# Performance work log

Hardware: AMD Instinct MI355X
Metric: run time of the kernel (lower is better)

Reference implementation:

```python
import jax, jax.numpy as jnp
import numpy as np

N = 10000      # nodes per graph
E = 160000     # random edges per graph (plus N self-loops)
IN_DIM = 4096
HID = 64       # num_hidden
H = 8          # heads
C = 5          # num_classes
SLOPE = 0.2    # LeakyReLU negative slope


def gat_conv(x, src, dst, W, al, ar, b, res_W=None):
    """DGL-style GATConv. x:(N,F) -> (N,H,D). Messages flow src->dst,
    edge softmax over in-edges of each dst node."""
    n = x.shape[0]
    h, d = al.shape
    feat = (x @ W).reshape(n, h, d)                      # (N,H,D)
    el = jnp.sum(feat * al, axis=-1)                     # (N,H)
    er = jnp.sum(feat * ar, axis=-1)                     # (N,H)
    e = jax.nn.leaky_relu(el[src] + er[dst], SLOPE)      # (E,H)
    emax = jax.ops.segment_max(e, dst, num_segments=n)   # (N,H) stable softmax
    ex = jnp.exp(e - emax[dst])
    denom = jax.ops.segment_sum(ex, dst, num_segments=n)
    alpha = ex / denom[dst]                              # (E,H)
    out = jax.ops.segment_sum(feat[src] * alpha[..., None], dst, num_segments=n)
    if res_W is not None:
        out = out + (x @ res_W).reshape(n, h, d)         # residual projection
    return out + b.reshape(h, d)


def encoder(x, src, dst, W0, al0, ar0, b0, W1, al1, ar1, b1):
    h0 = jax.nn.elu(gat_conv(x, src, dst, W0, al0, ar0, b0))   # (N,H,D)
    h0 = h0.reshape(h0.shape[0], -1)                           # flatten(1)
    return jax.nn.elu(gat_conv(h0, src, dst, W1, al1, ar1, b1))


def setup_inputs() -> dict:
    key = jax.random.key(0)
    ks = list(jax.random.split(key, 40))
    ki = iter(ks)

    def edges(k):
        k1, k2 = jax.random.split(k)
        loop = jnp.arange(N, dtype=jnp.int32)
        s = jnp.concatenate([jax.random.randint(k1, (E,), 0, N, dtype=jnp.int32), loop])
        d = jnp.concatenate([jax.random.randint(k2, (E,), 0, N, dtype=jnp.int32), loop])
        return s, d

    inp = {}
    for name in ("s0", "s1", "t"):
        s, d = edges(next(ki))
        inp[f"src_{name}"], inp[f"dst_{name}"] = s, d
    inp["features_s0"] = jax.random.normal(next(ki), (N, IN_DIM), jnp.float32)
    inp["features_s1"] = jax.random.normal(next(ki), (N, IN_DIM), jnp.float32)
    inp["features_t"]  = jax.random.normal(next(ki), (N, IN_DIM), jnp.float32)

    def lin(k, fan_in, fan_out):
        return jax.random.normal(k, (fan_in, fan_out), jnp.float32) / np.sqrt(fan_in)

    inp["W0"] = lin(next(ki), IN_DIM, H * HID)
    inp["al0"] = 0.1 * jax.random.normal(next(ki), (H, HID), jnp.float32)
    inp["ar0"] = 0.1 * jax.random.normal(next(ki), (H, HID), jnp.float32)
    inp["b0"] = jnp.zeros((H * HID,), jnp.float32)
    inp["W1"] = lin(next(ki), H * HID, H * HID)
    inp["al1"] = 0.1 * jax.random.normal(next(ki), (H, HID), jnp.float32)
    inp["ar1"] = 0.1 * jax.random.normal(next(ki), (H, HID), jnp.float32)
    inp["b1"] = jnp.zeros((H * HID,), jnp.float32)
    for k_idx in (0, 1):
        inp[f"Wc{k_idx}"] = lin(next(ki), H * HID, H * C)
        inp[f"alc{k_idx}"] = 0.1 * jax.random.normal(next(ki), (H, C), jnp.float32)
        inp[f"arc{k_idx}"] = 0.1 * jax.random.normal(next(ki), (H, C), jnp.float32)
        inp[f"bc{k_idx}"] = jnp.zeros((H * C,), jnp.float32)
        inp[f"rW{k_idx}"] = lin(next(ki), H * HID, H * C)
    inp["num_source"] = 2
    return inp


def reference(features_s0, features_s1, features_t,
              W0, al0, ar0, b0, W1, al1, ar1, b1,
              Wc0, alc0, arc0, bc0, rW0,
              Wc1, alc1, arc1, bc1, rW1,
              src_s0, dst_s0, src_s1, dst_s1, src_t, dst_t,
              num_source):
    enc_p = (W0, al0, ar0, b0, W1, al1, ar1, b1)
    cls_p = [(Wc0, alc0, arc0, bc0, rW0), (Wc1, alc1, arc1, bc1, rW1)]
    feats = [features_s0, features_s1]
    graphs = [(src_s0, dst_s0), (src_s1, dst_s1)]

    # shared-weight encoder on each source graph
    h_s = [encoder(feats[i], graphs[i][0], graphs[i][1], *enc_p)
           for i in range(num_source)]                    # each (N,H,HID)
    # per-source classifiers on their own graphs, mean over heads
    pred_s = []
    for i in range(num_source):
        Wc, alc, arc, bc, rW = cls_p[i]
        s, d = graphs[i]
        logits = gat_conv(h_s[i].reshape(N, -1), s, d, Wc, alc, arc, bc, res_W=rW)
        pred_s.append(logits.mean(axis=1))               # (N,C)
    emb_s = [h.reshape(N, -1) for h in h_s]

    # target: every source classifier applied to the target graph
    h_t = encoder(features_t, src_t, dst_t, *enc_p)
    pred_t = []
    for i in range(num_source):
        Wc, alc, arc, bc, rW = cls_p[i]
        logits = gat_conv(h_t.reshape(N, -1), src_t, dst_t, Wc, alc, arc, bc, res_W=rW)
        pred_t.append(logits.mean(axis=1))
    emb_t = h_t.reshape(N, -1)

    return (pred_s[0], pred_s[1], pred_t[0], pred_t[1], emb_s[0], emb_s[1], emb_t)
```

## Files before the change

kernel.cpp:

```cpp
#include <hip/hip_runtime.h>
#include <stdint.h>

typedef _Float16 f16;
typedef _Float16 f16x2 __attribute__((ext_vector_type(2)));
typedef _Float16 f16x8 __attribute__((ext_vector_type(8)));
typedef float f32x4 __attribute__((ext_vector_type(4)));

#define AS1 __attribute__((address_space(1)))
#define AS3 __attribute__((address_space(3)))

#define NN 10000
#define NP 10112
#define KK0 4096
#define FF 512

__global__ void k_count_b(const int* __restrict__ d0, const int* __restrict__ d1,
                          const int* __restrict__ d2, int E0, int E1, int E2,
                          int nb0, int nb1, int* __restrict__ deg){
  int b = blockIdx.x;
  const int* d; int Eg, base, lb;
  if (b < nb0){ d=d0; Eg=E0; base=0; lb=b; }
  else if (b < nb0+nb1){ d=d1; Eg=E1; base=NN; lb=b-nb0; }
  else { d=d2; Eg=E2; base=2*NN; lb=b-nb0-nb1; }
  int i = lb*256 + threadIdx.x;
  if (i < Eg) atomicAdd(&deg[base + d[i]], 1);
}

__global__ __launch_bounds__(1024) void k_scan_b(const int* __restrict__ deg_all,
    int* __restrict__ rowptr_all, int* __restrict__ cursor_all){
  int g = blockIdx.x;
  const int* deg = deg_all + g*NN;
  int* rowptr = rowptr_all + g*(NN+1);
  int* cursor = cursor_all + g*NN;
  __shared__ int ps[1024];
  int t = threadIdx.x;
  const int CH = 16;
  int i0 = t*CH;
  int sum = 0;
  for (int k=0;k<CH;k++){ int i=i0+k; if (i<NN) sum += deg[i]; }
  ps[t]=sum; __syncthreads();
  for (int off=1; off<1024; off<<=1){
    int v = (t>=off)? ps[t-off] : 0;
    __syncthreads();
    ps[t] += v;
    __syncthreads();
  }
  int run = ps[t]-sum;
  for (int k=0;k<CH;k++){
    int i=i0+k;
    if (i<=NN) rowptr[i]=run;
    if (i<NN){ cursor[i]=run; run += deg[i]; }
  }
}

__global__ void k_fill_b(const int* __restrict__ s0, const int* __restrict__ d0,
                         const int* __restrict__ s1, const int* __restrict__ d1,
                         const int* __restrict__ s2, const int* __restrict__ d2,
                         int E0, int E1, int E2, int nb0, int nb1,
                         int* __restrict__ cursor_all,
                         int* __restrict__ c0, int* __restrict__ c1, int* __restrict__ c2){
  int b = blockIdx.x;
  const int *s, *d; int Eg, lb; int* cur; int* col;
  if (b < nb0){ s=s0; d=d0; Eg=E0; lb=b; cur=cursor_all; col=c0; }
  else if (b < nb0+nb1){ s=s1; d=d1; Eg=E1; lb=b-nb0; cur=cursor_all+NN; col=c1; }
  else { s=s2; d=d2; Eg=E2; lb=b-nb0-nb1; cur=cursor_all+2*NN; col=c2; }
  int i = lb*256 + threadIdx.x;
  if (i >= Eg) return;
  int slot = atomicAdd(&cur[d[i]], 1);
  col[slot] = s[i];
}

__global__ void k_transpose_t(const float* __restrict__ W, f16* __restrict__ WT,
                              int K, int Nc){
  __shared__ float tile[32][33];
  int n0 = blockIdx.x*32, k0 = blockIdx.y*32;
  int tx = threadIdx.x, ty = threadIdx.y;
  #pragma unroll
  for (int i=0;i<32;i+=8)
    tile[ty+i][tx] = W[(long)(k0+ty+i)*Nc + n0+tx];
  __syncthreads();
  #pragma unroll
  for (int i=0;i<32;i+=8)
    WT[(long)(n0+ty+i)*K + k0+tx] = (f16)tile[tx][ty+i];
}

__global__ void k_pack_wc(const float* __restrict__ Wc, const float* __restrict__ rW,
                          f16* __restrict__ WT){
  int idx = blockIdx.x*256 + threadIdx.x;
  if (idx >= 128*512) return;
  int n = idx >> 9; int k = idx & 511;
  float v = 0.f;
  if (n < 40) v = Wc[k*40 + n];
  else if (n < 80) v = rW[k*40 + (n-40)];
  WT[idx] = (f16)v;
}

template<bool CVT>
__global__ __launch_bounds__(512,1) void k_gemmw(
    const void* __restrict__ A0v, const void* __restrict__ A1v, const void* __restrict__ A2v,
    f16* __restrict__ C0, f16* __restrict__ C1, f16* __restrict__ C2,
    const f16* __restrict__ B,
    const float* __restrict__ alp, const float* __restrict__ arp,
    float* __restrict__ elp, float* __restrict__ erp)
{
  constexpr int K = CVT ? KK0 : FF;
  constexpr int nt = K >> 6;
  __shared__ f16 lds[2][40960];

  const int nwg = gridDim.x;
  const int qd = nwg>>3, rd = nwg&7;
  const int xcd = blockIdx.x & 7, bx = blockIdx.x >> 3;
  const int wid = (xcd < rd ? xcd*(qd+1) : rd*(qd+1) + (xcd-rd)*qd) + bx;
  const int task = wid / 79;
  const int tr = wid - task*79;

  f16* C = task==0?C0:(task==1?C1:C2);

  const int t = threadIdx.x;
  const int wave = t >> 6, lane = t & 63;
  const int slot = (lane&7) ^ (lane>>3);
  const int arow0 = t >> 3;
  const int ak8 = t & 7;

  #define GLDSB(kt, buf) { \
    int ko = (kt)*64; \
    _Pragma("unroll") \
    for (int i=0;i<8;i++){ \
      int br = i*64 + wave*8 + (lane>>3); \
      __builtin_amdgcn_global_load_lds((const AS1 void*)(B + (long)br*K + ko + slot*8), \
          (AS3 void*)(&lds[buf][8192 + i*4096 + wave*512]), 16, 0, 0); \
    } }

  int abyte[2][8], bbyte[2][4];
  #pragma unroll
  for (int ks=0;ks<2;ks++){
    #pragma unroll
    for (int m=0;m<8;m++){
      int row = m*16 + (lane&15);
      abyte[ks][m] = row*128 + (((ks*4 + (lane>>4))*16) ^ ((row&7)<<4));
    }
    #pragma unroll
    for (int n=0;n<4;n++){
      int brow = wave*64 + n*16 + (lane&15);
      bbyte[ks][n] = 16384 + brow*128 + (((ks*4 + (lane>>4))*16) ^ ((brow&7)<<4));
    }
  }

  f32x4 zero4 = {0.f,0.f,0.f,0.f};
  f32x4 acc[8][4];
  #pragma unroll
  for (int m=0;m<8;m++)
    #pragma unroll
    for (int n=0;n<4;n++) acc[m][n] = zero4;

  #define MFMA_TILE(buf) { \
    const char* Ls = (const char*)&lds[buf][0]; \
    _Pragma("unroll") \
    for (int ks=0;ks<2;ks++){ \
      f16x8 bf[4]; \
      _Pragma("unroll") \
      for (int n=0;n<4;n++) bf[n] = *(const f16x8*)(Ls + bbyte[ks][n]); \
      _Pragma("unroll") \
      for (int m=0;m<8;m++){ \
        f16x8 af = *(const f16x8*)(Ls + abyte[ks][m]); \
        _Pragma("unroll") \
        for (int n=0;n<4;n++) \
          acc[m][n] = __builtin_amdgcn_mfma_f32_16x16x32_f16(af, bf[n], acc[m][n], 0, 0, 0); \
      } \
    } }

  int cur = 0;
  if constexpr (CVT){
    const float* Af = task==0?(const float*)A0v:(task==1?(const float*)A1v:(const float*)A2v);
    const float* gA[2];
    bool okA[2];
    #pragma unroll
    for (int s=0;s<2;s++){
      int grow = tr*128 + arow0 + s*64;
      okA[s] = grow < NN;
      gA[s] = Af + (long)(okA[s] ? grow : 0)*KK0 + ak8*8;
    }
    f32x4 arE[2][2];

    #define LOADA(kt) { \
      _Pragma("unroll") \
      for (int s=0;s<2;s++){ \
        arE[s][0] = *(const f32x4*)(gA[s] + (kt)*64); \
        arE[s][1] = *(const f32x4*)(gA[s] + (kt)*64 + 4); \
      } }
    #define WRITEA(buf) { \
      _Pragma("unroll") \
      for (int s=0;s<2;s++){ \
        int row = arow0 + s*64; \
        f16x8 v; \
        _Pragma("unroll") \
        for (int j=0;j<4;j++){ \
          v[j]   = okA[s] ? (f16)arE[s][0][j] : (f16)0.f; \
          v[4+j] = okA[s] ? (f16)arE[s][1][j] : (f16)0.f; \
        } \
        *(f16x8*)(&lds[buf][row*64 + ((ak8 ^ (arow0&7))*8)]) = v; \
      } }

    LOADA(0);
    __builtin_amdgcn_sched_barrier(0);
    GLDSB(0, 0);
    __builtin_amdgcn_sched_barrier(0);
    WRITEA(0);
    __builtin_amdgcn_sched_barrier(0);
    LOADA(1);
    __builtin_amdgcn_sched_barrier(0);
    asm volatile("s_waitcnt vmcnt(4) lgkmcnt(0)" ::: "memory");
    __builtin_amdgcn_s_barrier();

    for (int kt=0; kt<nt; kt++){
      if (kt+1 < nt){
        WRITEA(cur^1);
        __builtin_amdgcn_sched_barrier(0);
        GLDSB(kt+1, cur^1);
        __builtin_amdgcn_sched_barrier(0);
      }
      if (kt+2 < nt){
        LOADA(kt+2);
        __builtin_amdgcn_sched_barrier(0);
      }
      MFMA_TILE(cur);
      if (kt+1 < nt){
        __builtin_amdgcn_sched_barrier(0);
        if (kt+2 < nt)
          asm volatile("s_waitcnt vmcnt(4) lgkmcnt(0)" ::: "memory");
        else
          asm volatile("s_waitcnt vmcnt(0) lgkmcnt(0)" ::: "memory");
        __builtin_amdgcn_s_barrier();
      }
      cur ^= 1;
    }
    #undef LOADA
    #undef WRITEA
  } else {
    const f16* Ah = task==0?(const f16*)A0v:(task==1?(const f16*)A1v:(const f16*)A2v);
    const f16* Ab = Ah + (long)tr*128*K;
    const int r8 = lane>>3;

    #define GLDSA(kt, buf) { \
      _Pragma("unroll") \
      for (int s=0;s<2;s++){ \
        int arow = wave*8 + r8 + s*64; \
        __builtin_amdgcn_global_load_lds((const AS1 void*)(Ab + (long)arow*K + (kt)*64 + slot*8), \
            (AS3 void*)(&lds[buf][s*4096 + wave*512]), 16, 0, 0); \
      } }

    GLDSA(0, 0);
    GLDSB(0, 0);
    __syncthreads();
    for (int kt=0; kt<nt; kt++){
      if (kt+1 < nt){
        GLDSA(kt+1, cur^1);
        GLDSB(kt+1, cur^1);
      }
      MFMA_TILE(cur);
      __syncthreads();
      cur ^= 1;
    }
    #undef GLDSA
  }
  #undef GLDSB
  #undef MFMA_TILE

  #pragma unroll
  for (int m=0;m<8;m++){
    int row0 = tr*128 + m*16 + ((lane>>4)<<2);
    #pragma unroll
    for (int n=0;n<4;n++){
      int col = wave*64 + n*16 + (lane&15);
      #pragma unroll
      for (int q2=0;q2<4;q2++)
        C[(long)(row0+q2)*FF + col] = (f16)acc[m][n][q2];
    }
  }

  {
    const int head = wave;
    const float* alh = alp + head*64;
    const float* arh = arp + head*64;
    float alv[4], arv[4];
    #pragma unroll
    for (int n=0;n<4;n++){ int d = n*16 + (lane&15); alv[n]=alh[d]; arv[n]=arh[d]; }
    float* elo = elp + (long)task*NN*8;
    float* ero = erp + (long)task*NN*8;
    #pragma unroll
    for (int m=0;m<8;m++){
      float e0,e1,e2,e3,r0,r1,r2,r3;
      #pragma unroll
      for (int qq=0;qq<4;qq++){
        float e=0.f, rr=0.f;
        #pragma unroll
        for (int n=0;n<4;n++){ e += acc[m][n][qq]*alv[n]; rr += acc[m][n][qq]*arv[n]; }
        #pragma unroll
        for (int off=1; off<16; off<<=1){ e += __shfl_xor(e, off); rr += __shfl_xor(rr, off); }
        if (qq==0){e0=e;r0=rr;} else if (qq==1){e1=e;r1=rr;} else if (qq==2){e2=e;r2=rr;} else {e3=e;r3=rr;}
      }
      int qq = lane&15;
      if (qq < 4){
        int node = tr*128 + m*16 + ((lane>>4)<<2) + qq;
        if (node < NN){
          float ev = qq==0?e0:(qq==1?e1:(qq==2?e2:e3));
          float rv = qq==0?r0:(qq==1?r1:(qq==2?r2:r3));
          long o = (long)node*8 + head;
          elo[o] = ev;
          ero[o] = rv;
        }
      }
    }
  }
}

struct GemmTasks { const f16* A[4]; const f16* B[4]; f16* C[4]; };

__global__ __launch_bounds__(256,3) void k_gemmb(GemmTasks p, int ntpb, int ntn,
                                                 int Nc, int K){
  __shared__ f16 lds[2][12288];
  const int bid = blockIdx.x;
  const int task = bid / ntpb;
  const int orig = bid - task*ntpb;
  const int q = ntpb >> 3, r = ntpb & 7;
  const int xcd = orig & 7, bx = orig >> 3;
  const int wid = (xcd < r ? xcd*(q+1) : r*(q+1) + (xcd-r)*q) + bx;
  const int tr = wid / ntn, tc = wid - tr*ntn;

  const f16* A = p.A[task];
  const f16* B = p.B[task];
  f16* C = p.C[task];

  const int t = threadIdx.x;
  const int wave = t >> 6, lane = t & 63;
  const int wr = wave >> 1, wc = wave & 1;

  const f16* Ab = A + (long)tr*64*K;
  const f16* Bb = B + (long)tc*128*K;

  const int slot = (lane&7) ^ (lane>>3);
  const int rbase = wave*8 + (lane>>3);

  f32x4 zero4 = {0.f,0.f,0.f,0.f};
  f32x4 acc[2][4];
  #pragma unroll
  for (int m=0;m<2;m++)
    #pragma unroll
    for (int n=0;n<4;n++) acc[m][n] = zero4;

  int abyte[2][2], bbyte[2][4];
  #pragma unroll
  for (int ks=0;ks<2;ks++){
    #pragma unroll
    for (int m=0;m<2;m++){
      int row = wr*32 + m*16 + (lane&15);
      abyte[ks][m] = row*128 + (((ks*4 + (lane>>4))*16) ^ ((row&7)<<4));
    }
    #pragma unroll
    for (int n=0;n<4;n++){
      int brow = wc*64 + n*16 + (lane&15);
      bbyte[ks][n] = 8192 + brow*128 + (((ks*4 + (lane>>4))*16) ^ ((brow&7)<<4));
    }
  }

  const int nt = K >> 6;
  int cur = 0;

  #pragma unroll
  for (int i=0;i<2;i++)
    __builtin_amdgcn_global_load_lds((const AS1 void*)(Ab + (i*32+rbase)*K + slot*8),
        (AS3 void*)(&lds[0][i*2048 + wave*512]), 16, 0, 0);
  #pragma unroll
  for (int i=0;i<4;i++)
    __builtin_amdgcn_global_load_lds((const AS1 void*)(Bb + (i*32+rbase)*K + slot*8),
        (AS3 void*)(&lds[0][4096 + i*2048 + wave*512]), 16, 0, 0);
  __syncthreads();

  for (int kt=0; kt<nt; kt++){
    if (kt+1 < nt){
      int ko = (kt+1)<<6;
      #pragma unroll
      for (int i=0;i<2;i++)
        __builtin_amdgcn_global_load_lds((const AS1 void*)(Ab + ko + (i*32+rbase)*K + slot*8),
            (AS3 void*)(&lds[cur^1][i*2048 + wave*512]), 16, 0, 0);
      #pragma unroll
      for (int i=0;i<4;i++)
        __builtin_amdgcn_global_load_lds((const AS1 void*)(Bb + ko + (i*32+rbase)*K + slot*8),
            (AS3 void*)(&lds[cur^1][4096 + i*2048 + wave*512]), 16, 0, 0);
    }
    const char* Ls = (const char*)&lds[cur][0];
    #pragma unroll
    for (int ks=0;ks<2;ks++){
      f16x8 af[2], bf[4];
      #pragma unroll
      for (int m=0;m<2;m++) af[m] = *(const f16x8*)(Ls + abyte[ks][m]);
      #pragma unroll
      for (int n=0;n<4;n++) bf[n] = *(const f16x8*)(Ls + bbyte[ks][n]);
      #pragma unroll
      for (int m=0;m<2;m++)
        #pragma unroll
        for (int n=0;n<4;n++)
          acc[m][n] = __builtin_amdgcn_mfma_f32_16x16x32_f16(af[m], bf[n], acc[m][n], 0, 0, 0);
    }
    __syncthreads();
    cur ^= 1;
  }

  #pragma unroll
  for (int m=0;m<2;m++){
    int row0 = tr*64 + wr*32 + m*16 + ((lane>>4)<<2);
    #pragma unroll
    for (int n=0;n<4;n++){
      int col = tc*128 + wc*64 + n*16 + (lane&15);
      #pragma unroll
      for (int q2=0;q2<4;q2++)
        C[(long)(row0+q2)*Nc + col] = (f16)acc[m][n][q2];
    }
  }
}

#define MAXD 128

struct AggArgs {
  const int* rp[3]; const int* cs[3];
  const float* el; const float* er;
  const f16* feat[3];
  const float* bias;
  f16* outH[3];
  float* outF[3];
};

__global__ __launch_bounds__(256) void k_agg_b(AggArgs a){
  int b = blockIdx.x;
  int g = b / NN, n = b - g*NN;
  const int* rowptr = a.rp[g];
  const int* colsrc = a.cs[g];
  const float* el = a.el + (long)g*NN*8;
  const f16* featH = a.feat[g];
  int t = threadIdx.x;
  __shared__ float sm[MAXD*8];
  __shared__ int   scol[MAXD];
  __shared__ float red[256];
  __shared__ float inv[8];
  __shared__ float ern[8];
  if (t < 8) ern[t] = a.er[((long)g*NN+n)*8+t];
  __syncthreads();
  int j0 = rowptr[n], deg = rowptr[n+1]-j0;
  {
    int h = t & 7;
    float dsum = 0.f;
    for (int jj = t>>3; jj < deg; jj += 32){
      int s = colsrc[j0+jj];
      float v = el[s*8+h] + ern[h];
      v = (v>0.f)? v : 0.2f*v;
      float ex = __expf(v);
      dsum += ex;
      if (jj < MAXD){
        sm[jj*8+h] = ex;
        if (h==0) scol[jj] = s;
      }
    }
    red[t] = dsum; __syncthreads();
    if (t<128) red[t] += red[t+128]; __syncthreads();
    if (t<64)  red[t] += red[t+64];  __syncthreads();
    if (t<32)  red[t] += red[t+32];  __syncthreads();
    if (t<16)  red[t] += red[t+16];  __syncthreads();
    if (t<8)   inv[t] = 1.0f / (red[t] + red[t+8]);
    __syncthreads();
  }
  int h = t >> 5;
  int c = t*2;
  float a0=0.f, a1=0.f;
  float ivh = inv[h];
  for (int jj=0; jj<deg; jj++){
    int s; float ex;
    if (jj < MAXD){ s = scol[jj]; ex = sm[jj*8+h]; }
    else {
      s = colsrc[j0+jj];
      float v = el[s*8+h] + ern[h];
      v = (v>0.f)? v : 0.2f*v;
      ex = __expf(v);
    }
    float alpha = ex * ivh;
    f16x2 f = *(const f16x2*)(featH + (long)s*FF + c);
    a0 += alpha*(float)f[0];
    a1 += alpha*(float)f[1];
  }
  a0 += a.bias[c]; a1 += a.bias[c+1];
  a0 = (a0>0.f)? a0 : __expf(a0)-1.f;
  a1 = (a1>0.f)? a1 : __expf(a1)-1.f;
  f16x2 o; o[0]=(f16)a0; o[1]=(f16)a1;
  *(f16x2*)(a.outH[g] + (long)n*FF + c) = o;
  float* oF = a.outF[g];
  if (oF){
    oF[(long)n*FF + c]     = a0;
    oF[(long)n*FF + c + 1] = a1;
  }
}

__global__ void k_elerc_b(const f16* __restrict__ fc,
    const float* __restrict__ alc0, const float* __restrict__ arc0,
    const float* __restrict__ alc1, const float* __restrict__ arc1,
    float* __restrict__ el, float* __restrict__ er){
  int idx = blockIdx.x*256 + threadIdx.x;
  if (idx >= 4*NN*8) return;
  int ti = idx / (NN*8);
  int rem = idx - ti*NN*8;
  int n = rem>>3, hh = rem&7;
  const f16* featc = fc + (long)ti*NP*128;
  const float* al = (ti&1) ? alc1 : alc0;
  const float* ar_ = (ti&1) ? arc1 : arc0;
  float a=0.f, bsum=0.f;
  #pragma unroll
  for (int cc=0; cc<5; cc++){
    float v = (float)featc[(long)n*128 + hh*5 + cc];
    a += v*al[hh*5+cc];
    bsum += v*ar_[hh*5+cc];
  }
  el[idx]=a; er[idx]=bsum;
}

struct ClsArgs {
  const int* rp[3]; const int* cs[3];
  const float* el; const float* er;
  const f16* fc;
  const float* bc[2];
  float* pred;
};

__global__ __launch_bounds__(64) void k_cls_b(ClsArgs a){
  int b = blockIdx.x;
  int ti = b / NN, n = b - ti*NN;
  int g = ti<2 ? ti : 2;
  int ci = ti&1;
  const int* rowptr = a.rp[g];
  const int* colsrc = a.cs[g];
  const float* el = a.el + (long)ti*NN*8;
  const f16* featc = a.fc + (long)ti*NP*128;
  const float* bc = a.bc[ci];
  float* pred = a.pred + (long)ti*5*NN;
  int l = threadIdx.x;
  __shared__ float sm[MAXD*8];
  __shared__ int   scol[MAXD];
  __shared__ float inv[8];
  __shared__ float ern[8];
  __shared__ float lg[40];
  if (l<8) ern[l] = a.er[((long)ti*NN+n)*8+l];
  __syncthreads();
  int j0 = rowptr[n], deg = rowptr[n+1]-j0;
  {
    int h = l & 7;
    float dsum = 0.f;
    for (int jj = l>>3; jj < deg; jj += 8){
      int s = colsrc[j0+jj];
      float v = el[s*8+h] + ern[h];
      v = (v>0.f)? v : 0.2f*v;
      float ex = __expf(v);
      dsum += ex;
      if (jj < MAXD){
        sm[jj*8+h] = ex;
        if (h==0) scol[jj] = s;
      }
    }
    dsum += __shfl_xor(dsum, 8);
    dsum += __shfl_xor(dsum, 16);
    dsum += __shfl_xor(dsum, 32);
    if (l<8) inv[l] = 1.0f/dsum;
  }
  __syncthreads();
  if (l<40){
    int h = l/5;
    float ivh = inv[h];
    float acc = 0.f;
    for (int jj=0; jj<deg; jj++){
      int s; float ex;
      if (jj < MAXD){ s = scol[jj]; ex = sm[jj*8+h]; }
      else {
        s = colsrc[j0+jj];
        float v = el[s*8+h] + ern[h];
        v = (v>0.f)? v : 0.2f*v;
        ex = __expf(v);
      }
      acc += ex*ivh * (float)featc[(long)s*128 + l];
    }
    acc += (float)featc[(long)n*128 + 40 + l];
    acc += bc[l];
    lg[l] = acc;
  }
  __syncthreads();
  if (l<5){
    float p=0.f;
    #pragma unroll
    for (int h=0;h<8;h++) p += lg[h*5+l];
    pred[(long)n*5 + l] = p*0.125f;
  }
}

extern "C" void kernel_launch(void* const* d_in, const int* in_sizes, int n_in,
                              void* d_out, int out_size, void* d_ws, size_t ws_size,
                              hipStream_t stream){
  const int* srcs[3] = {(const int*)d_in[0], (const int*)d_in[2], (const int*)d_in[4]};
  const int* dsts[3] = {(const int*)d_in[1], (const int*)d_in[3], (const int*)d_in[5]};
  int E[3] = {in_sizes[0], in_sizes[2], in_sizes[4]};
  const float* X[3] = {(const float*)d_in[6], (const float*)d_in[7], (const float*)d_in[8]};
  const float* W0  = (const float*)d_in[9];
  const float* al0 = (const float*)d_in[10];
  const float* ar0 = (const float*)d_in[11];
  const float* b0  = (const float*)d_in[12];
  const float* W1  = (const float*)d_in[13];
  const float* al1 = (const float*)d_in[14];
  const float* ar1 = (const float*)d_in[15];
  const float* b1  = (const float*)d_in[16];
  const float* Wcv[2] = {(const float*)d_in[17], (const float*)d_in[22]};
  const float* alc[2] = {(const float*)d_in[18], (const float*)d_in[23]};
  const float* arc[2] = {(const float*)d_in[19], (const float*)d_in[24]};
  const float* bcv[2] = {(const float*)d_in[20], (const float*)d_in[25]};
  const float* rWv[2] = {(const float*)d_in[21], (const float*)d_in[26]};

  float* out = (float*)d_out;
  float* embOut[3] = {out+200000, out+200000+(long)NN*FF, out+200000+2L*NN*FF};

  char* w = (char*)d_ws;
  size_t off = 0;
  auto alloc = [&](size_t bytes)->void*{
    void* p = (void*)(w + off);
    off += (bytes + 255) & ~((size_t)255);
    return p;
  };
  f16* W0T = (f16*)alloc((size_t)FF*KK0*2);
  f16* W1T = (f16*)alloc((size_t)FF*FF*2);
  f16* WcT[2] = {(f16*)alloc(128*512*2), (f16*)alloc(128*512*2)};
  f16* feat0H[3], *h0H[3], *feat1H[3], *embH[3];
  for (int g=0;g<3;g++) feat0H[g] = (f16*)alloc((size_t)NP*FF*2);
  for (int g=0;g<3;g++) h0H[g]    = (f16*)alloc((size_t)NP*FF*2);
  for (int g=0;g<3;g++) feat1H[g] = (f16*)alloc((size_t)NP*FF*2);
  for (int g=0;g<3;g++) embH[g]   = (f16*)alloc((size_t)NP*FF*2);
  f16* featc = (f16*)alloc((size_t)4*NP*128*2);
  float* el_e = (float*)alloc((size_t)3*NN*8*4);
  float* er_e = (float*)alloc((size_t)3*NN*8*4);
  float* el_c = (float*)alloc((size_t)4*NN*8*4);
  float* er_c = (float*)alloc((size_t)4*NN*8*4);
  int* deg    = (int*)alloc((size_t)3*NN*4);
  int* cursor = (int*)alloc((size_t)3*NN*4);
  int* rowptr = (int*)alloc((size_t)3*(NN+1)*4);
  int* colsrc[3];
  for (int g=0;g<3;g++) colsrc[g] = (int*)alloc((size_t)E[g]*4);
  (void)ws_size; (void)n_in; (void)out_size;

  int nb[3] = {(E[0]+255)/256, (E[1]+255)/256, (E[2]+255)/256};
  hipMemsetAsync(deg, 0, (size_t)3*NN*4, stream);
  k_count_b<<<nb[0]+nb[1]+nb[2], 256, 0, stream>>>(dsts[0], dsts[1], dsts[2],
      E[0], E[1], E[2], nb[0], nb[1], deg);
  k_scan_b<<<3, 1024, 0, stream>>>(deg, rowptr, cursor);
  k_fill_b<<<nb[0]+nb[1]+nb[2], 256, 0, stream>>>(srcs[0], dsts[0], srcs[1], dsts[1],
      srcs[2], dsts[2], E[0], E[1], E[2], nb[0], nb[1], cursor,
      colsrc[0], colsrc[1], colsrc[2]);

  k_transpose_t<<<dim3(FF/32, KK0/32), dim3(32,8), 0, stream>>>(W0, W0T, KK0, FF);
  k_transpose_t<<<dim3(FF/32, FF/32), dim3(32,8), 0, stream>>>(W1, W1T, FF, FF);
  k_pack_wc<<<(128*512+255)/256, 256, 0, stream>>>(Wcv[0], rWv[0], WcT[0]);
  k_pack_wc<<<(128*512+255)/256, 256, 0, stream>>>(Wcv[1], rWv[1], WcT[1]);

  const int* rp[3] = {rowptr, rowptr+(NN+1), rowptr+2*(NN+1)};

  k_gemmw<true><<<237, 512, 0, stream>>>(X[0], X[1], X[2],
      feat0H[0], feat0H[1], feat0H[2], W0T, al0, ar0, el_e, er_e);
  {
    AggArgs a;
    for (int g=0;g<3;g++){ a.rp[g]=rp[g]; a.cs[g]=colsrc[g]; a.feat[g]=feat0H[g];
                           a.outH[g]=h0H[g]; a.outF[g]=nullptr; }
    a.el = el_e; a.er = er_e; a.bias = b0;
    k_agg_b<<<3*NN, 256, 0, stream>>>(a);
  }

  k_gemmw<false><<<237, 512, 0, stream>>>(h0H[0], h0H[1], h0H[2],
      feat1H[0], feat1H[1], feat1H[2], W1T, al1, ar1, el_e, er_e);
  {
    AggArgs a;
    for (int g=0;g<3;g++){ a.rp[g]=rp[g]; a.cs[g]=colsrc[g]; a.feat[g]=feat1H[g];
                           a.outH[g]=embH[g]; a.outF[g]=embOut[g]; }
    a.el = el_e; a.er = er_e; a.bias = b1;
    k_agg_b<<<3*NN, 256, 0, stream>>>(a);
  }

  {
    GemmTasks p;
    const int tg[4] = {0,1,2,2};
    for (int i=0;i<4;i++){ p.A[i]=embH[tg[i]]; p.B[i]=WcT[i&1]; p.C[i]=featc + (long)i*NP*128; }
    k_gemmb<<<4*158, 256, 0, stream>>>(p, 158, 1, 128, FF);
  }
  k_elerc_b<<<(4*NN*8+255)/256, 256, 0, stream>>>(featc, alc[0], arc[0], alc[1], arc[1], el_c, er_c);
  {
    ClsArgs a;
    for (int g=0;g<3;g++){ a.rp[g]=rp[g]; a.cs[g]=colsrc[g]; }
    a.el = el_c; a.er = er_c; a.fc = featc;
    a.bc[0] = bcv[0]; a.bc[1] = bcv[1];
    a.pred = out;
    k_cls_b<<<4*NN, 64, 0, stream>>>(a);
  }
}
```

Baseline: 538.5 us.

## Interleave GEMM loads with MFMA halves and unroll aggregation gathers by four

The CVT GEMM main loop now splits each k-tile into two MFMA halves. Half of the B-tile global-to-LDS loads and the A prefetch are issued between the halves, and s_setprio raises wave priority during the MFMA phases to overlap memory issue with compute. The edge aggregation kernels gain a fast path for degree at most MAXD that unrolls the gather loop by four, which exposes more independent loads. That path also moves the softmax normalization out of the loop into a single multiply. The extra code path and the scheduling barriers add complexity and may raise register pressure.

New measurement: 512.2 us. -4.9%, faster.

```diff
diff --git a/kernel.cpp b/kernel.cpp
--- a/kernel.cpp
+++ b/kernel.cpp
@@ -122,14 +122,15 @@
   const int arow0 = t >> 3;
   const int ak8 = t & 7;
 
-  #define GLDSB(kt, buf) { \
+  #define GLDSB_H(kt, buf, half) { \
     int ko = (kt)*64; \
     _Pragma("unroll") \
-    for (int i=0;i<8;i++){ \
+    for (int i=(half)*4; i<(half)*4+4; i++){ \
       int br = i*64 + wave*8 + (lane>>3); \
       __builtin_amdgcn_global_load_lds((const AS1 void*)(B + (long)br*K + ko + slot*8), \
           (AS3 void*)(&lds[buf][8192 + i*4096 + wave*512]), 16, 0, 0); \
     } }
+  #define GLDSB(kt, buf) { GLDSB_H(kt, buf, 0); GLDSB_H(kt, buf, 1); }
 
   int abyte[2][8], bbyte[2][4];
   #pragma unroll
@@ -153,20 +154,17 @@
     #pragma unroll
     for (int n=0;n<4;n++) acc[m][n] = zero4;
 
-  #define MFMA_TILE(buf) { \
+  #define MFMA_KS(buf, ks) { \
     const char* Ls = (const char*)&lds[buf][0]; \
+    f16x8 bf[4]; \
     _Pragma("unroll") \
-    for (int ks=0;ks<2;ks++){ \
-      f16x8 bf[4]; \
+    for (int n=0;n<4;n++) bf[n] = *(const f16x8*)(Ls + bbyte[ks][n]); \
+    _Pragma("unroll") \
+    for (int m=0;m<8;m++){ \
+      f16x8 af = *(const f16x8*)(Ls + abyte[ks][m]); \
       _Pragma("unroll") \
-      for (int n=0;n<4;n++) bf[n] = *(const f16x8*)(Ls + bbyte[ks][n]); \
-      _Pragma("unroll") \
-      for (int m=0;m<8;m++){ \
-        f16x8 af = *(const f16x8*)(Ls + abyte[ks][m]); \
-        _Pragma("unroll") \
-        for (int n=0;n<4;n++) \
-          acc[m][n] = __builtin_amdgcn_mfma_f32_16x16x32_f16(af, bf[n], acc[m][n], 0, 0, 0); \
-      } \
+      for (int n=0;n<4;n++) \
+        acc[m][n] = __builtin_amdgcn_mfma_f32_16x16x32_f16(af, bf[n], acc[m][n], 0, 0, 0); \
     } }
 
   int cur = 0;
@@ -211,26 +209,38 @@
     __builtin_amdgcn_sched_barrier(0);
     asm volatile("s_waitcnt vmcnt(4) lgkmcnt(0)" ::: "memory");
     __builtin_amdgcn_s_barrier();
+    __builtin_amdgcn_sched_barrier(0);
 
     for (int kt=0; kt<nt; kt++){
       if (kt+1 < nt){
+        GLDSB_H(kt+1, cur^1, 0);
+        __builtin_amdgcn_sched_barrier(0);
         WRITEA(cur^1);
         __builtin_amdgcn_sched_barrier(0);
-        GLDSB(kt+1, cur^1);
+      }
+      __builtin_amdgcn_s_setprio(1);
+      MFMA_KS(cur, 0);
+      __builtin_amdgcn_s_setprio(0);
+      __builtin_amdgcn_sched_barrier(0);
+      if (kt+1 < nt){
+        GLDSB_H(kt+1, cur^1, 1);
         __builtin_amdgcn_sched_barrier(0);
       }
       if (kt+2 < nt){
         LOADA(kt+2);
         __builtin_amdgcn_sched_barrier(0);
       }
-      MFMA_TILE(cur);
+      __builtin_amdgcn_s_setprio(1);
+      MFMA_KS(cur, 1);
+      __builtin_amdgcn_s_setprio(0);
+      __builtin_amdgcn_sched_barrier(0);
       if (kt+1 < nt){
-        __builtin_amdgcn_sched_barrier(0);
         if (kt+2 < nt)
           asm volatile("s_waitcnt vmcnt(4) lgkmcnt(0)" ::: "memory");
         else
           asm volatile("s_waitcnt vmcnt(0) lgkmcnt(0)" ::: "memory");
         __builtin_amdgcn_s_barrier();
+        __builtin_amdgcn_sched_barrier(0);
       }
       cur ^= 1;
     }
@@ -257,14 +267,16 @@
         GLDSA(kt+1, cur^1);
         GLDSB(kt+1, cur^1);
       }
-      MFMA_TILE(cur);
+      MFMA_KS(cur, 0);
+      MFMA_KS(cur, 1);
       __syncthreads();
       cur ^= 1;
     }
     #undef GLDSA
   }
   #undef GLDSB
-  #undef MFMA_TILE
+  #undef GLDSB_H
+  #undef MFMA_KS
 
   #pragma unroll
   for (int m=0;m<8;m++){
@@ -446,46 +458,91 @@
   if (t < 8) ern[t] = a.er[((long)g*NN+n)*8+t];
   __syncthreads();
   int j0 = rowptr[n], deg = rowptr[n+1]-j0;
-  {
-    int h = t & 7;
-    float dsum = 0.f;
-    for (int jj = t>>3; jj < deg; jj += 32){
-      int s = colsrc[j0+jj];
-      float v = el[s*8+h] + ern[h];
-      v = (v>0.f)? v : 0.2f*v;
-      float ex = __expf(v);
-      dsum += ex;
-      if (jj < MAXD){
+  int h2 = t >> 5;
+  int c = t*2;
+  float a0=0.f, a1=0.f;
+
+  if (deg <= MAXD){
+    {
+      int h = t & 7;
+      float dsum = 0.f;
+      for (int jj = t>>3; jj < deg; jj += 32){
+        int s = colsrc[j0+jj];
+        float v = el[s*8+h] + ern[h];
+        v = (v>0.f)? v : 0.2f*v;
+        float ex = __expf(v);
+        dsum += ex;
         sm[jj*8+h] = ex;
         if (h==0) scol[jj] = s;
       }
-    }
-    red[t] = dsum; __syncthreads();
-    if (t<128) red[t] += red[t+128]; __syncthreads();
-    if (t<64)  red[t] += red[t+64];  __syncthreads();
-    if (t<32)  red[t] += red[t+32];  __syncthreads();
-    if (t<16)  red[t] += red[t+16];  __syncthreads();
-    if (t<8)   inv[t] = 1.0f / (red[t] + red[t+8]);
-    __syncthreads();
-  }
-  int h = t >> 5;
-  int c = t*2;
-  float a0=0.f, a1=0.f;
-  float ivh = inv[h];
-  for (int jj=0; jj<deg; jj++){
-    int s; float ex;
-    if (jj < MAXD){ s = scol[jj]; ex = sm[jj*8+h]; }
-    else {
-      s = colsrc[j0+jj];
-      float v = el[s*8+h] + ern[h];
-      v = (v>0.f)? v : 0.2f*v;
-      ex = __expf(v);
-    }
-    float alpha = ex * ivh;
-    f16x2 f = *(const f16x2*)(featH + (long)s*FF + c);
-    a0 += alpha*(float)f[0];
-    a1 += alpha*(float)f[1];
-  }
+      red[t] = dsum; __syncthreads();
+      if (t<128) red[t] += red[t+128]; __syncthreads();
+      if (t<64)  red[t] += red[t+64];  __syncthreads();
+      if (t<32)  red[t] += red[t+32];  __syncthreads();
+      if (t<16)  red[t] += red[t+16];  __syncthreads();
+      if (t<8)   inv[t] = 1.0f / (red[t] + red[t+8]);
+      __syncthreads();
+    }
+    float ivh = inv[h2];
+    int jj = 0;
+    for (; jj+4<=deg; jj+=4){
+      int s0=scol[jj], s1=scol[jj+1], s2=scol[jj+2], s3=scol[jj+3];
+      float x0=sm[(jj+0)*8+h2], x1=sm[(jj+1)*8+h2], x2=sm[(jj+2)*8+h2], x3=sm[(jj+3)*8+h2];
+      f16x2 f0 = *(const f16x2*)(featH + (long)s0*FF + c);
+      f16x2 f1 = *(const f16x2*)(featH + (long)s1*FF + c);
+      f16x2 f2 = *(const f16x2*)(featH + (long)s2*FF + c);
+      f16x2 f3 = *(const f16x2*)(featH + (long)s3*FF + c);
+      a0 += x0*(float)f0[0] + x1*(float)f1[0] + x2*(float)f2[0] + x3*(float)f3[0];
+      a1 += x0*(float)f0[1] + x1*(float)f1[1] + x2*(float)f2[1] + x3*(float)f3[1];
+    }
+    for (; jj<deg; jj++){
+      int s = scol[jj];
+      float x = sm[jj*8+h2];
+      f16x2 f = *(const f16x2*)(featH + (long)s*FF + c);
+      a0 += x*(float)f[0];
+      a1 += x*(float)f[1];
+    }
+    a0 *= ivh; a1 *= ivh;
+  } else {
+    {
+      int h = t & 7;
+      float dsum = 0.f;
+      for (int jj = t>>3; jj < deg; jj += 32){
+        int s = colsrc[j0+jj];
+        float v = el[s*8+h] + ern[h];
+        v = (v>0.f)? v : 0.2f*v;
+        float ex = __expf(v);
+        dsum += ex;
+        if (jj < MAXD){
+          sm[jj*8+h] = ex;
+          if (h==0) scol[jj] = s;
+        }
+      }
+      red[t] = dsum; __syncthreads();
+      if (t<128) red[t] += red[t+128]; __syncthreads();
+      if (t<64)  red[t] += red[t+64];  __syncthreads();
+      if (t<32)  red[t] += red[t+32];  __syncthreads();
+      if (t<16)  red[t] += red[t+16];  __syncthreads();
+      if (t<8)   inv[t] = 1.0f / (red[t] + red[t+8]);
+      __syncthreads();
+    }
+    float ivh = inv[h2];
+    for (int jj=0; jj<deg; jj++){
+      int s; float ex;
+      if (jj < MAXD){ s = scol[jj]; ex = sm[jj*8+h2]; }
+      else {
+        s = colsrc[j0+jj];
+        float v = el[s*8+h2] + ern[h2];
+        v = (v>0.f)? v : 0.2f*v;
+        ex = __expf(v);
+      }
+      float alpha = ex * ivh;
+      f16x2 f = *(const f16x2*)(featH + (long)s*FF + c);
+      a0 += alpha*(float)f[0];
+      a1 += alpha*(float)f[1];
+    }
+  }
+
   a0 += a.bias[c]; a1 += a.bias[c+1];
   a0 = (a0>0.f)? a0 : __expf(a0)-1.f;
   a1 = (a1>0.f)? a1 : __expf(a1)-1.f;
@@ -548,44 +605,87 @@
   if (l<8) ern[l] = a.er[((long)ti*NN+n)*8+l];
   __syncthreads();
   int j0 = rowptr[n], deg = rowptr[n+1]-j0;
-  {
-    int h = l & 7;
-    float dsum = 0.f;
-    for (int jj = l>>3; jj < deg; jj += 8){
-      int s = colsrc[j0+jj];
-      float v = el[s*8+h] + ern[h];
-      v = (v>0.f)? v : 0.2f*v;
-      float ex = __expf(v);
-      dsum += ex;
-      if (jj < MAXD){
+
+  if (deg <= MAXD){
+    {
+      int h = l & 7;
+      float dsum = 0.f;
+      for (int jj = l>>3; jj < deg; jj += 8){
+        int s = colsrc[j0+jj];
+        float v = el[s*8+h] + ern[h];
+        v = (v>0.f)? v : 0.2f*v;
+        float ex = __expf(v);
+        dsum += ex;
         sm[jj*8+h] = ex;
         if (h==0) scol[jj] = s;
       }
-    }
-    dsum += __shfl_xor(dsum, 8);
-    dsum += __shfl_xor(dsum, 16);
-    dsum += __shfl_xor(dsum, 32);
-    if (l<8) inv[l] = 1.0f/dsum;
-  }
-  __syncthreads();
-  if (l<40){
-    int h = l/5;
-    float ivh = inv[h];
-    float acc = 0.f;
-    for (int jj=0; jj<deg; jj++){
-      int s; float ex;
-      if (jj < MAXD){ s = scol[jj]; ex = sm[jj*8+h]; }
-      else {
-        s = colsrc[j0+jj];
+      dsum += __shfl_xor(dsum, 8);
+      dsum += __shfl_xor(dsum, 16);
+      dsum += __shfl_xor(dsum, 32);
+      if (l<8) inv[l] = 1.0f/dsum;
+    }
+    __syncthreads();
+    if (l<40){
+      int h = l/5;
+      float ivh = inv[h];
+      float acc = 0.f;
+      int jj = 0;
+      for (; jj+4<=deg; jj+=4){
+        int s0=scol[jj], s1=scol[jj+1], s2=scol[jj+2], s3=scol[jj+3];
+        float x0=sm[(jj+0)*8+h], x1=sm[(jj+1)*8+h], x2=sm[(jj+2)*8+h], x3=sm[(jj+3)*8+h];
+        float v0=(float)featc[(long)s0*128 + l];
+        float v1=(float)featc[(long)s1*128 + l];
+        float v2=(float)featc[(long)s2*128 + l];
+        float v3=(float)featc[(long)s3*128 + l];
+        acc += x0*v0 + x1*v1 + x2*v2 + x3*v3;
+      }
+      for (; jj<deg; jj++)
+        acc += sm[jj*8+h] * (float)featc[(long)scol[jj]*128 + l];
+      acc *= ivh;
+      acc += (float)featc[(long)n*128 + 40 + l];
+      acc += bc[l];
+      lg[l] = acc;
+    }
+  } else {
+    {
+      int h = l & 7;
+      float dsum = 0.f;
+      for (int jj = l>>3; jj < deg; jj += 8){
+        int s = colsrc[j0+jj];
         float v = el[s*8+h] + ern[h];
         v = (v>0.f)? v : 0.2f*v;
-        ex = __expf(v);
-      }
-      acc += ex*ivh * (float)featc[(long)s*128 + l];
-    }
-    acc += (float)featc[(long)n*128 + 40 + l];
-    acc += bc[l];
-    lg[l] = acc;
+        float ex = __expf(v);
+        dsum += ex;
+        if (jj < MAXD){
+          sm[jj*8+h] = ex;
+          if (h==0) scol[jj] = s;
+        }
+      }
+      dsum += __shfl_xor(dsum, 8);
+      dsum += __shfl_xor(dsum, 16);
+      dsum += __shfl_xor(dsum, 32);
+      if (l<8) inv[l] = 1.0f/dsum;
+    }
+    __syncthreads();
+    if (l<40){
+      int h = l/5;
+      float ivh = inv[h];
+      float acc = 0.f;
+      for (int jj=0; jj<deg; jj++){
+        int s; float ex;
+        if (jj < MAXD){ s = scol[jj]; ex = sm[jj*8+h]; }
+        else {
+          s = colsrc[j0+jj];
+          float v = el[s*8+h] + ern[h];
+          v = (v>0.f)? v : 0.2f*v;
+          ex = __expf(v);
+        }
+        acc += ex*ivh * (float)featc[(long)s*128 + l];
+      }
+      acc += (float)featc[(long)n*128 + 40 + l];
+      acc += bc[l];
+      lg[l] = acc;
+    }
   }
   __syncthreads();
   if (l<5){
```
